# Kernel optimization log

Hardware: AMD Instinct MI355X
Metric: run time of the kernel (lower is better)

## Reference

```python
import jax, jax.numpy as jnp
import numpy as np

EPS = 1e-5


def setup_inputs() -> dict:
    key = jax.random.key(0)
    ks = jax.random.split(key, 10)
    B, C, H, W = 4, 256, 64, 64
    x = jax.random.normal(ks[0], (B, C, H, W), dtype=jnp.float32)
    s = 1.0 / np.sqrt(C)
    inp = {
        "x": x,
        "gn_w": jnp.ones((C,), jnp.float32),
        "gn_b": jnp.zeros((C,), jnp.float32),
        "wq": jax.random.normal(ks[1], (C, C), jnp.float32) * s,
        "bq": jnp.zeros((C,), jnp.float32),
        "wk": jax.random.normal(ks[2], (C, C), jnp.float32) * s,
        "bk": jnp.zeros((C,), jnp.float32),
        "wv": jax.random.normal(ks[3], (C, C), jnp.float32) * s,
        "bv": jnp.zeros((C,), jnp.float32),
        "wo": jax.random.normal(ks[4], (C, C), jnp.float32) * s,
        "bo": jnp.zeros((C,), jnp.float32),
    }
    return inp


def _forward(x, gn_w, gn_b, wq, bq, wk, bk, wv, bv, wo, bo):
    B, C, H, W = x.shape
    G = C // 2  # num_groups = channels // 2 -> 2 channels per group
    # GroupNorm
    xg = x.reshape(B, G, C // G, H, W)
    mu = jnp.mean(xg, axis=(2, 3, 4), keepdims=True)
    var = jnp.var(xg, axis=(2, 3, 4), keepdims=True)
    hn = ((xg - mu) * jax.lax.rsqrt(var + EPS)).reshape(B, C, H, W)
    hn = hn * gn_w[None, :, None, None] + gn_b[None, :, None, None]
    # tokens: (B, N, C), N = H*W
    h = hn.transpose(0, 2, 3, 1).reshape(B, H * W, C)
    q = h @ wq.T + bq
    k = h @ wk.T + bk
    v = h @ wv.T + bv
    # full NxN attention, scaled by C^-0.5 (as in original)
    scores = jnp.einsum("bnc,bmc->bnm", q, k) * (C ** -0.5)
    attn = jax.nn.softmax(scores, axis=-1)
    h2 = jnp.einsum("bnm,bmc->bnc", attn, v)  # (B, N, C)
    # faithful replication of the original's layout-scrambling reshape:
    # (B,N,C) -> (B,H,W,C) -> permute (B,C,H,W) -> reshape (B,HW,C)
    h2 = h2.reshape(B, H, W, C).transpose(0, 3, 1, 2).reshape(B, H * W, C)
    out = (h2 @ wo.T + bo).reshape(B, C, H, W)
    return x + out


def reference(x, gn_w, gn_b, wq, bq, wk, bk, wv, bv, wo, bo):
    return _forward(x, gn_w, gn_b, wq, bq, wk, bk, wv, bv, wo, bo)
```

## Files before the change

### kernel.cpp

```cpp
#include <hip/hip_runtime.h>

typedef unsigned short u16;
typedef unsigned int   u32;
typedef __attribute__((ext_vector_type(8)))  short short8;
typedef __attribute__((ext_vector_type(4)))  float f32x4;
typedef __attribute__((ext_vector_type(16))) float f32x16;

#define DI __device__ __forceinline__

DI u16 f2bf(float f){
  u32 u = __builtin_bit_cast(u32, f);
  u += 0x7fffu + ((u >> 16) & 1u);
  return (u16)(u >> 16);
}

DI void gl_lds16(const void* g, void* l){
  __builtin_amdgcn_global_load_lds((const __attribute__((address_space(1))) void*)g,
                                   (__attribute__((address_space(3))) void*)l, 16, 0, 0);
}

DI f32x4 mfma16(short8 a, short8 b, f32x4 c){
  return __builtin_amdgcn_mfma_f32_16x16x32_bf16(a, b, c, 0, 0, 0);
}
DI f32x16 mfma32(short8 a, short8 b, f32x16 c){
  return __builtin_amdgcn_mfma_f32_32x32x16_bf16(a, b, c, 0, 0, 0);
}
DI f32x16 z16(){
  f32x16 v;
  #pragma unroll
  for (int i=0;i<16;i++) v[i]=0.f;
  return v;
}

union U8 { u32 u[4]; short8 s; };

#define OFF_WBF   0u
#define OFF_STATS (512u<<10)
#define OFF_HTOK  (1u<<20)
#define OFF_Q     ((1u<<20) + (8u<<20))
#define OFF_K     ((1u<<20) + (16u<<20))
#define OFF_VT    ((1u<<20) + (24u<<20))
#define OFF_H2T   OFF_Q
#define OFF_PART  ((1u<<20) + (32u<<20))
#define OFF_ML    ((1u<<20) + (96u<<20))

__global__ void k_prep(const float* w0, const float* w1, const float* w2, const float* w3, u16* wbf){
  const float* src = (blockIdx.y==0)?w0:(blockIdx.y==1)?w1:(blockIdx.y==2)?w2:w3;
  u16* d = wbf + blockIdx.y*65536;
  int i = (blockIdx.x*256 + threadIdx.x)*4;
  float4 v = *(const float4*)(src + i);
  u32 lo = (u32)f2bf(v.x) | ((u32)f2bf(v.y)<<16);
  u32 hi = (u32)f2bf(v.z) | ((u32)f2bf(v.w)<<16);
  *(uint2*)(d + i) = make_uint2(lo, hi);
}

__global__ void k_gnstats(const float* x, float2* stats){
  int bg = blockIdx.x;
  const float* p = x + (size_t)bg*8192;
  float s = 0.f, ss = 0.f;
  #pragma unroll
  for (int i=0;i<8;i++){
    float4 v = *(const float4*)(p + threadIdx.x*4 + i*1024);
    s  += v.x+v.y+v.z+v.w;
    ss += v.x*v.x + v.y*v.y + v.z*v.z + v.w*v.w;
  }
  #pragma unroll
  for (int off=1; off<64; off<<=1){ s += __shfl_xor(s, off, 64); ss += __shfl_xor(ss, off, 64); }
  __shared__ float as[4], aq[4];
  int w = threadIdx.x>>6;
  if ((threadIdx.x&63)==0){ as[w]=s; aq[w]=ss; }
  __syncthreads();
  if (threadIdx.x==0){
    s = as[0]+as[1]+as[2]+as[3]; ss = aq[0]+aq[1]+aq[2]+aq[3];
    float mu = s * (1.f/8192.f);
    float var = ss * (1.f/8192.f) - mu*mu;
    stats[bg] = make_float2(mu, rsqrtf(var + 1e-5f));
  }
}

__global__ void k_gnapply(const float* x, const float* gw, const float* gb,
                          const float2* stats, u16* htok){
  __shared__ u16 tile[64*256];
  int b = blockIdx.y, n0 = blockIdx.x*64, t = threadIdx.x;
  const float* xb = x + (size_t)b*1048576;
  #pragma unroll
  for (int p=0;p<4;p++){
    int c = p*64 + (t>>2);
    float2 st = stats[b*128 + (c>>1)];
    float scl = st.y * gw[c];
    float off = gb[c] - st.x*scl;
    const float* src = xb + (size_t)c*4096 + n0 + (t&3)*16;
    #pragma unroll
    for (int u2=0;u2<4;u2++){
      float4 v = *(const float4*)(src + u2*4);
      float vv[4] = {v.x,v.y,v.z,v.w};
      #pragma unroll
      for (int j=0;j<4;j++){
        int n = (t&3)*16 + u2*4 + j;
        int addr = n*512 + ((c*2) ^ ((n&7)<<4));
        *(u16*)((char*)tile + addr) = f2bf(vv[j]*scl + off);
      }
    }
  }
  __syncthreads();
  int n = t>>2, seg = t&3;
  char* dst = (char*)(htok + ((size_t)(b*4096 + n0 + n)*256 + seg*64));
  #pragma unroll
  for (int i=0;i<8;i++){
    int boff = n*512 + (((seg*128) + i*16) ^ ((n&7)<<4));
    *(uint4*)(dst + i*16) = *(const uint4*)((const char*)tile + boff);
  }
}

__global__ __launch_bounds__(256,2) void k_qkv(const u16* htok, const u16* wbf,
    const float* bq, const float* bk, const float* bv,
    u16* qo, u16* ko, u16* vt){
  __shared__ u16 lds_a[64*256];
  const int t = threadIdx.x, row0 = blockIdx.x*64;
  const int w = t>>6, l = t&63, lo = l&15, hi = l>>4;
  {
    const char* Ab = (const char*)htok + (size_t)row0*512;
    #pragma unroll
    for (int i=0;i<8;i++){
      int row = w*16 + i*2 + (l>>5);
      gl_lds16(Ab + row*512 + (((l&31)*16) ^ ((row&7)<<4)), lds_a + w*4096 + i*512);
    }
    __syncthreads();
  }
  auto compute = [&](const u16* W, f32x4 acc[4][4]){
    #pragma unroll
    for (int i=0;i<4;i++)
      #pragma unroll
      for (int j=0;j<4;j++) acc[i][j] = (f32x4){0.f,0.f,0.f,0.f};
    const char* Wb = (const char*)W;
    #pragma unroll
    for (int dk=0; dk<4; dk++){
      #pragma unroll
      for (int s=0;s<2;s++){
        short8 af[4], bf[4];
        #pragma unroll
        for (int cf=0;cf<4;cf++){
          int col = w*64 + cf*16 + lo;
          bf[cf] = *(const short8*)(Wb + (size_t)col*512 + dk*128 + s*64 + hi*16);
        }
        #pragma unroll
        for (int rg=0;rg<4;rg++){
          int row = rg*16 + lo;
          af[rg] = *(const short8*)((const char*)lds_a + row*512 + ((dk*128 + s*64 + hi*16) ^ ((row&7)<<4)));
        }
        #pragma unroll
        for (int rg=0;rg<4;rg++)
          #pragma unroll
          for (int cf=0;cf<4;cf++)
            acc[rg][cf] = mfma16(af[rg], bf[cf], acc[rg][cf]);
      }
    }
  };
  f32x4 acc[4][4];
  compute(wbf, acc);
  #pragma unroll
  for (int rg=0;rg<4;rg++)
    #pragma unroll
    for (int cf=0;cf<4;cf++){
      int col = w*64 + cf*16 + lo;
      float bs = bq[col];
      #pragma unroll
      for (int r=0;r<4;r++){
        int grow = row0 + rg*16 + hi*4 + r;
        qo[(size_t)grow*256 + col] = f2bf((acc[rg][cf][r] + bs)*0.09016844f);
      }
    }
  compute(wbf + 65536, acc);
  #pragma unroll
  for (int rg=0;rg<4;rg++)
    #pragma unroll
    for (int cf=0;cf<4;cf++){
      int col = w*64 + cf*16 + lo;
      float bs = bk[col];
      #pragma unroll
      for (int r=0;r<4;r++){
        int grow = row0 + rg*16 + hi*4 + r;
        ko[(size_t)grow*256 + col] = f2bf(acc[rg][cf][r] + bs);
      }
    }
  compute(wbf + 2*65536, acc);
  __syncthreads();
  #pragma unroll
  for (int rg=0;rg<4;rg++)
    #pragma unroll
    for (int cf=0;cf<4;cf++){
      int col = w*64 + cf*16 + lo;
      float bs = bv[col];
      ushort4 pk;
      pk.x = f2bf(acc[rg][cf][0]+bs); pk.y = f2bf(acc[rg][cf][1]+bs);
      pk.z = f2bf(acc[rg][cf][2]+bs); pk.w = f2bf(acc[rg][cf][3]+bs);
      int rl = rg*16 + hi*4;
      int addr = col*128 + ((rl*2) ^ ((col&7)<<4));
      *(ushort4*)((char*)lds_a + addr) = pk;
    }
  __syncthreads();
  {
    int b = row0 >> 12, nb = row0 & 4095;
    #pragma unroll
    for (int p=0;p<8;p++){
      int c = p*32 + (t>>3), i = t&7;
      uint4 vd = *(const uint4*)((const char*)lds_a + c*128 + ((i*16) ^ ((c&7)<<4)));
      *(uint4*)((char*)vt + ((size_t)(b*256 + c)*4096 + nb)*2 + i*16) = vd;
    }
  }
}

__global__ __launch_bounds__(256,2) void k_out(const u16* h2t, const u16* wo,
    const float* bo, const float* x, float* out){
  __shared__ u16 lds_a[64*256];
  const int t = threadIdx.x, row0 = blockIdx.x*64;
  const int w = t>>6, l = t&63, lo = l&15, hi = l>>4;
  {
    const char* Ab = (const char*)h2t + (size_t)row0*512;
    #pragma unroll
    for (int i=0;i<8;i++){
      int row = w*16 + i*2 + (l>>5);
      gl_lds16(Ab + row*512 + (((l&31)*16) ^ ((row&7)<<4)), lds_a + w*4096 + i*512);
    }
    __syncthreads();
  }
  f32x4 acc[4][4];
  #pragma unroll
  for (int i=0;i<4;i++)
    #pragma unroll
    for (int j=0;j<4;j++) acc[i][j] = (f32x4){0.f,0.f,0.f,0.f};
  const char* Wb = (const char*)wo;
  #pragma unroll
  for (int dk=0; dk<4; dk++){
    #pragma unroll
    for (int s=0;s<2;s++){
      short8 af[4], bf[4];
      #pragma unroll
      for (int cf=0;cf<4;cf++){
        int col = w*64 + cf*16 + lo;
        bf[cf] = *(const short8*)(Wb + (size_t)col*512 + dk*128 + s*64 + hi*16);
      }
      #pragma unroll
      for (int rg=0;rg<4;rg++){
        int row = rg*16 + lo;
        af[rg] = *(const short8*)((const char*)lds_a + row*512 + ((dk*128 + s*64 + hi*16) ^ ((row&7)<<4)));
      }
      #pragma unroll
      for (int rg=0;rg<4;rg++)
        #pragma unroll
        for (int cf=0;cf<4;cf++)
          acc[rg][cf] = mfma16(af[rg], bf[cf], acc[rg][cf]);
    }
  }
  #pragma unroll
  for (int rg=0;rg<4;rg++)
    #pragma unroll
    for (int cf=0;cf<4;cf++){
      int col = w*64 + cf*16 + lo;
      float bs = bo[col];
      #pragma unroll
      for (int r=0;r<4;r++){
        size_t flat = (size_t)(row0 + rg*16 + hi*4 + r)*256 + col;
        out[flat] = x[flat] + acc[rg][cf][r] + bs;
      }
    }
}

__global__ __launch_bounds__(512,2) void k_attn(const u16* q, const u16* k,
                                                const u16* vt, u16* part, float2* ml){
  __shared__ char smem[131072];
  const int t = threadIdx.x, w = t>>6, l = t&63;
  const int lq = l&31, h = l>>5;
  const int bid = blockIdx.x;
  const int x = bid&7, idx = bid>>3;
  const int combo = x*2 + (idx&1);
  const int b = combo>>2, ks = combo&3, qt = idx>>1;

  const char* kg = (const char*)k  + ((size_t)b*4096 + (size_t)ks*1024)*512;
  const char* vg = (const char*)vt + (size_t)b*2097152 + (size_t)ks*2048;

  short8 qf[16];
  {
    const char* qrow = (const char*)q + ((size_t)b*4096 + qt*256 + w*32 + lq)*512;
    #pragma unroll
    for (int dk=0;dk<16;dk++) qf[dk] = *(const short8*)(qrow + dk*32 + h*16);
  }

  f32x16 O[8];
  #pragma unroll
  for (int ct=0;ct<8;ct++) O[ct] = z16();
  float m_run = -1e30f, l_run = 0.f;

  auto stage = [&](int sub){
    char* kd = smem + (sub&3)*16384;
    char* vd = smem + 65536 + (sub&3)*16384;
    #pragma unroll
    for (int j=0;j<2;j++){
      int key = w*4 + j*2 + h;
      gl_lds16(kg + (size_t)(sub*32 + key)*512 + (((l&31)*16) ^ ((key&7)<<4)),
               kd + (w*2+j)*1024);
    }
    #pragma unroll
    for (int j=0;j<2;j++){
      int c = w*32 + j*16 + (l>>2);
      gl_lds16(vg + (size_t)c*8192 + sub*64 + (((l&3)*16) ^ (((l>>3)&3)<<4)),
               vd + (w*2+j)*1024);
    }
  };

  auto qkt = [&](int sub, f32x16& S){
    const char* kbuf = smem + (sub&3)*16384;
    S = z16();
    #pragma unroll
    for (int dk=0;dk<16;dk++){
      short8 kf = *(const short8*)(kbuf + (size_t)lq*512 + ((dk*32 + h*16) ^ ((lq&7)<<4)));
      S = mfma32(kf, qf[dk], S);
    }
  };

  auto smpv = [&](int sub, const f32x16& S){
    const char* vbuf = smem + 65536 + (sub&3)*16384;
    float pmax = S[0];
    #pragma unroll
    for (int r=1;r<16;r++) pmax = fmaxf(pmax, S[r]);
    pmax = fmaxf(pmax, __shfl_xor(pmax, 32, 64));
    if (__any(pmax > m_run + 8.f)){
      float mn = fmaxf(m_run, pmax);
      float sclq = exp2f(m_run - mn);
      m_run = mn;
      l_run *= sclq;
      #pragma unroll
      for (int r=0;r<16;r++){
        float sr = __shfl(sclq, (r&3)+8*(r>>2)+4*h, 64);
        #pragma unroll
        for (int ct=0;ct<8;ct++) O[ct][r] *= sr;
      }
    }
    float p[16]; float ps = 0.f;
    #pragma unroll
    for (int r=0;r<16;r++){ p[r] = exp2f(S[r] - m_run); ps += p[r]; }
    l_run += ps + __shfl_xor(ps, 32, 64);
    u32 pk[8];
    #pragma unroll
    for (int j=0;j<8;j++){
      u32 u0 = __builtin_bit_cast(u32, p[2*j]);
      u32 u1 = __builtin_bit_cast(u32, p[2*j+1]);
      pk[j] = (u1 & 0xffff0000u) | (u0 >> 16);
    }
    #pragma unroll
    for (int kc=0;kc<2;kc++){
      u32 sA = h ? pk[4*kc]   : pk[4*kc+2];
      u32 sB = h ? pk[4*kc+1] : pk[4*kc+3];
      u32 xA = __shfl_xor(sA, 32, 64);
      u32 xB = __shfl_xor(sB, 32, 64);
      U8 pa;
      pa.u[0] = h ? xA : pk[4*kc];
      pa.u[1] = h ? xB : pk[4*kc+1];
      pa.u[2] = h ? pk[4*kc+2] : xA;
      pa.u[3] = h ? pk[4*kc+3] : xB;
      #pragma unroll
      for (int ct=0;ct<8;ct++){
        short8 vb = *(const short8*)(vbuf + (size_t)(ct*32+lq)*64 + ((kc*32 + h*16) ^ (((lq>>1)&3)<<4)));
        O[ct] = mfma32(pa.s, vb, O[ct]);
      }
    }
  };

  f32x16 SA, SB;
  stage(0); stage(1); stage(2);
  __syncthreads();
  qkt(0, SA);
  for (int it=0; it<30; it+=2){
    stage(it+3);
    qkt(it+1, SB);
    smpv(it, SA);
    __syncthreads();
    if (it+4 < 32) stage(it+4);
    qkt(it+2, SA);
    smpv(it+1, SB);
    __syncthreads();
  }
  qkt(31, SB);
  smpv(30, SA);
  smpv(31, SB);

  if (h == 0)
    ml[(size_t)combo*4096 + qt*256 + w*32 + lq] = make_float2(m_run, l_run);
  u16* otile = (u16*)smem;
  char* pbase = (char*)part + ((size_t)combo*4096 + (size_t)qt*256)*512;
  #pragma unroll
  for (int rd=0; rd<2; ++rd){
    __syncthreads();
    if ((w>>2) == rd){
      int wl = w&3;
      #pragma unroll
      for (int ct=0;ct<8;ct++)
        #pragma unroll
        for (int r=0;r<16;r++){
          int row = wl*32 + (r&3) + 8*(r>>2) + 4*h;
          otile[row*256 + ct*32 + lq] = f2bf(O[ct][r]);
        }
    }
    __syncthreads();
    const char* sb2 = (const char*)smem;
    char* gb2 = pbase + (size_t)rd*65536;
    #pragma unroll
    for (int j=0;j<8;j++)
      *(uint4*)(gb2 + t*16 + (size_t)j*8192) = *(const uint4*)(sb2 + t*16 + (size_t)j*8192);
  }
}

__global__ __launch_bounds__(256,2) void k_combine(const u16* part, const float2* ml, u16* h2t){
  __shared__ u16 tile[64*256];
  const int t = threadIdx.x, b = blockIdx.y, n0 = blockIdx.x*64;
  const int n = t>>2, cc = (t&3)*64;
  const int gn = n0 + n;
  float2 st[4]; float ms = -1e30f;
  #pragma unroll
  for (int ksi=0;ksi<4;ksi++){ st[ksi] = ml[(size_t)(b*4+ksi)*4096 + gn]; ms = fmaxf(ms, st[ksi].x); }
  float wn[4]; float denom = 0.f;
  #pragma unroll
  for (int ksi=0;ksi<4;ksi++){ wn[ksi] = exp2f(st[ksi].x - ms); denom += wn[ksi]*st[ksi].y; }
  float inv = 1.f/denom;
  #pragma unroll
  for (int ksi=0;ksi<4;ksi++) wn[ksi] *= inv;
  float acc[64];
  #pragma unroll
  for (int j=0;j<64;j++) acc[j] = 0.f;
  #pragma unroll
  for (int ksi=0;ksi<4;ksi++){
    const u16* src = part + ((size_t)(b*4+ksi)*4096 + gn)*256 + cc;
    float wv = wn[ksi];
    #pragma unroll
    for (int j8=0;j8<8;j8++){
      short8 v = *(const short8*)(src + j8*8);
      #pragma unroll
      for (int e=0;e<8;e++){
        u32 uu = ((u32)(u16)v[e])<<16;
        acc[j8*8+e] += wv * __builtin_bit_cast(float, uu);
      }
    }
  }
  char* tb = (char*)tile;
  #pragma unroll
  for (int j=0;j<32;j++){
    u32 pkv = ((u32)f2bf(acc[2*j+1])<<16) | f2bf(acc[2*j]);
    *(u32*)(tb + n*512 + ((cc*2 + j*4) ^ ((n&7)<<4))) = pkv;
  }
  __syncthreads();
  {
    const char* tbc = (const char*)tile;
    u32 outw[32];
    #pragma unroll
    for (int j=0;j<32;j++){
      u16 v0 = *(const u16*)(tbc + (2*j  )*512 + ((t*2) ^ (((2*j  )&7)<<4)));
      u16 v1 = *(const u16*)(tbc + (2*j+1)*512 + ((t*2) ^ (((2*j+1)&7)<<4)));
      outw[j] = ((u32)v1<<16) | v0;
    }
    char* dst = (char*)h2t + ((size_t)(b*256 + t)*4096 + n0)*2;
    #pragma unroll
    for (int j=0;j<8;j++){
      uint4 vv; vv.x = outw[4*j]; vv.y = outw[4*j+1]; vv.z = outw[4*j+2]; vv.w = outw[4*j+3];
      *(uint4*)(dst + j*16) = vv;
    }
  }
}

extern "C" void kernel_launch(void* const* d_in, const int* in_sizes, int n_in,
                              void* d_out, int out_size, void* d_ws, size_t ws_size,
                              hipStream_t stream) {
  const float* x    = (const float*)d_in[0];
  const float* gn_w = (const float*)d_in[1];
  const float* gn_b = (const float*)d_in[2];
  const float* wq   = (const float*)d_in[3];
  const float* bq   = (const float*)d_in[4];
  const float* wk   = (const float*)d_in[5];
  const float* bk   = (const float*)d_in[6];
  const float* wv   = (const float*)d_in[7];
  const float* bv   = (const float*)d_in[8];
  const float* wo   = (const float*)d_in[9];
  const float* bo   = (const float*)d_in[10];
  float* out = (float*)d_out;
  char* ws = (char*)d_ws;

  u16*    wbf   = (u16*)(ws + OFF_WBF);
  float2* stats = (float2*)(ws + OFF_STATS);
  u16*    htok  = (u16*)(ws + OFF_HTOK);
  u16*    qb    = (u16*)(ws + OFF_Q);
  u16*    kb    = (u16*)(ws + OFF_K);
  u16*    vt    = (u16*)(ws + OFF_VT);
  u16*    h2t   = (u16*)(ws + OFF_H2T);
  u16*    part  = (u16*)(ws + OFF_PART);
  float2* ml    = (float2*)(ws + OFF_ML);

  k_prep   <<<dim3(64,4), 256, 0, stream>>>(wq, wk, wv, wo, wbf);
  k_gnstats<<<512,        256, 0, stream>>>(x, stats);
  k_gnapply<<<dim3(64,4), 256, 0, stream>>>(x, gn_w, gn_b, stats, htok);
  k_qkv    <<<256,        256, 0, stream>>>(htok, wbf, bq, bk, bv, qb, kb, vt);
  k_attn   <<<256,        512, 0, stream>>>(qb, kb, vt, part, ml);
  k_combine<<<dim3(64,4), 256, 0, stream>>>(part, ml, h2t);
  k_out    <<<256,        256, 0, stream>>>(h2t, wbf + 3*65536, bo, x, out);
}
```

Before: 185.6 us.

## Restructure attention K/V pipeline into double-buffered 64-key tiles, merge prep kernels

```diff
diff --git a/kernel.cpp b/kernel.cpp
--- a/kernel.cpp
+++ b/kernel.cpp
@@ -44,18 +44,21 @@
 #define OFF_PART  ((1u<<20) + (32u<<20))
 #define OFF_ML    ((1u<<20) + (96u<<20))
 
-__global__ void k_prep(const float* w0, const float* w1, const float* w2, const float* w3, u16* wbf){
-  const float* src = (blockIdx.y==0)?w0:(blockIdx.y==1)?w1:(blockIdx.y==2)?w2:w3;
-  u16* d = wbf + blockIdx.y*65536;
-  int i = (blockIdx.x*256 + threadIdx.x)*4;
-  float4 v = *(const float4*)(src + i);
-  u32 lo = (u32)f2bf(v.x) | ((u32)f2bf(v.y)<<16);
-  u32 hi = (u32)f2bf(v.z) | ((u32)f2bf(v.w)<<16);
-  *(uint2*)(d + i) = make_uint2(lo, hi);
-}
-
-__global__ void k_gnstats(const float* x, float2* stats){
-  int bg = blockIdx.x;
+__global__ void k_prepstats(const float* wq, const float* wk, const float* wv, const float* wo,
+                            u16* wbf, const float* x, float2* stats){
+  const int bid = blockIdx.x;
+  if (bid < 256){
+    const int wi = bid >> 6;
+    const float* src = (wi==0)?wq:(wi==1)?wk:(wi==2)?wv:wo;
+    u16* d = wbf + wi*65536;
+    int i = ((bid&63)*256 + threadIdx.x)*4;
+    float4 v = *(const float4*)(src + i);
+    u32 lo = (u32)f2bf(v.x) | ((u32)f2bf(v.y)<<16);
+    u32 hi = (u32)f2bf(v.z) | ((u32)f2bf(v.w)<<16);
+    *(uint2*)(d + i) = make_uint2(lo, hi);
+    return;
+  }
+  const int bg = bid - 256;
   const float* p = x + (size_t)bg*8192;
   float s = 0.f, ss = 0.f;
   #pragma unroll
@@ -291,35 +294,27 @@
   for (int ct=0;ct<8;ct++) O[ct] = z16();
   float m_run = -1e30f, l_run = 0.f;
 
-  auto stage = [&](int sub){
-    char* kd = smem + (sub&3)*16384;
-    char* vd = smem + 65536 + (sub&3)*16384;
-    #pragma unroll
-    for (int j=0;j<2;j++){
-      int key = w*4 + j*2 + h;
-      gl_lds16(kg + (size_t)(sub*32 + key)*512 + (((l&31)*16) ^ ((key&7)<<4)),
-               kd + (w*2+j)*1024);
-    }
-    #pragma unroll
-    for (int j=0;j<2;j++){
-      int c = w*32 + j*16 + (l>>2);
-      gl_lds16(vg + (size_t)c*8192 + sub*64 + (((l&3)*16) ^ (((l>>3)&3)<<4)),
-               vd + (w*2+j)*1024);
+  auto stage = [&](int ti, int buf){
+    #pragma unroll
+    for (int sub=0; sub<2; ++sub){
+      char* kd = smem + buf*32768 + sub*16384;
+      char* vd = smem + 65536 + buf*32768 + sub*16384;
+      #pragma unroll
+      for (int j=0;j<2;j++){
+        int key = w*4 + j*2 + h;
+        gl_lds16(kg + (size_t)(ti*64 + sub*32 + key)*512 + (((l&31)*16) ^ ((key&7)<<4)),
+                 kd + (w*2+j)*1024);
+      }
+      #pragma unroll
+      for (int j=0;j<2;j++){
+        int c = w*32 + j*16 + (l>>2);
+        gl_lds16(vg + (size_t)c*8192 + ti*128 + sub*64 + (((l&3)*16) ^ (((l>>3)&3)<<4)),
+                 vd + (w*2+j)*1024);
+      }
     }
   };
 
-  auto qkt = [&](int sub, f32x16& S){
-    const char* kbuf = smem + (sub&3)*16384;
-    S = z16();
-    #pragma unroll
-    for (int dk=0;dk<16;dk++){
-      short8 kf = *(const short8*)(kbuf + (size_t)lq*512 + ((dk*32 + h*16) ^ ((lq&7)<<4)));
-      S = mfma32(kf, qf[dk], S);
-    }
-  };
-
-  auto smpv = [&](int sub, const f32x16& S){
-    const char* vbuf = smem + 65536 + (sub&3)*16384;
+  auto smpv = [&](const f32x16& S, const char* vbuf){
     float pmax = S[0];
     #pragma unroll
     for (int r=1;r<16;r++) pmax = fmaxf(pmax, S[r]);
@@ -358,31 +353,43 @@
       pa.u[1] = h ? xB : pk[4*kc+1];
       pa.u[2] = h ? pk[4*kc+2] : xA;
       pa.u[3] = h ? pk[4*kc+3] : xB;
+      __builtin_amdgcn_s_setprio(1);
       #pragma unroll
       for (int ct=0;ct<8;ct++){
         short8 vb = *(const short8*)(vbuf + (size_t)(ct*32+lq)*64 + ((kc*32 + h*16) ^ (((lq>>1)&3)<<4)));
         O[ct] = mfma32(pa.s, vb, O[ct]);
       }
+      __builtin_amdgcn_s_setprio(0);
     }
   };
 
-  f32x16 SA, SB;
-  stage(0); stage(1); stage(2);
+  stage(0, 0);
   __syncthreads();
-  qkt(0, SA);
-  for (int it=0; it<30; it+=2){
-    stage(it+3);
-    qkt(it+1, SB);
-    smpv(it, SA);
+
+  for (int tile=0; tile<16; ++tile){
+    const int cur = tile&1;
+    if (tile < 15) stage(tile+1, cur^1);
+    const char* kbuf0 = smem + cur*32768;
+    const char* kbuf1 = kbuf0 + 16384;
+    const char* vbuf0 = smem + 65536 + cur*32768;
+    const char* vbuf1 = vbuf0 + 16384;
+
+    f32x16 S0 = z16(), S1 = z16();
+    __builtin_amdgcn_s_setprio(1);
+    #pragma unroll
+    for (int dk=0;dk<16;dk++){
+      int dby = (dk*32 + h*16) ^ ((lq&7)<<4);
+      short8 k0 = *(const short8*)(kbuf0 + (size_t)lq*512 + dby);
+      short8 k1 = *(const short8*)(kbuf1 + (size_t)lq*512 + dby);
+      S0 = mfma32(k0, qf[dk], S0);
+      S1 = mfma32(k1, qf[dk], S1);
+    }
+    __builtin_amdgcn_s_setprio(0);
+
+    smpv(S0, vbuf0);
+    smpv(S1, vbuf1);
     __syncthreads();
-    if (it+4 < 32) stage(it+4);
-    qkt(it+2, SA);
-    smpv(it+1, SB);
-    __syncthreads();
-  }
-  qkt(31, SB);
-  smpv(30, SA);
-  smpv(31, SB);
+  }
 
   if (h == 0)
     ml[(size_t)combo*4096 + qt*256 + w*32 + lq] = make_float2(m_run, l_run);
@@ -493,11 +500,10 @@
   u16*    part  = (u16*)(ws + OFF_PART);
   float2* ml    = (float2*)(ws + OFF_ML);
 
-  k_prep   <<<dim3(64,4), 256, 0, stream>>>(wq, wk, wv, wo, wbf);
-  k_gnstats<<<512,        256, 0, stream>>>(x, stats);
-  k_gnapply<<<dim3(64,4), 256, 0, stream>>>(x, gn_w, gn_b, stats, htok);
-  k_qkv    <<<256,        256, 0, stream>>>(htok, wbf, bq, bk, bv, qb, kb, vt);
-  k_attn   <<<256,        512, 0, stream>>>(qb, kb, vt, part, ml);
-  k_combine<<<dim3(64,4), 256, 0, stream>>>(part, ml, h2t);
-  k_out    <<<256,        256, 0, stream>>>(h2t, wbf + 3*65536, bo, x, out);
-}
+  k_prepstats<<<768,      256, 0, stream>>>(wq, wk, wv, wo, wbf, x, stats);
+  k_gnapply  <<<dim3(64,4), 256, 0, stream>>>(x, gn_w, gn_b, stats, htok);
+  k_qkv      <<<256,      256, 0, stream>>>(htok, wbf, bq, bk, bv, qb, kb, vt);
+  k_attn     <<<256,      512, 0, stream>>>(qb, kb, vt, part, ml);
+  k_combine  <<<dim3(64,4), 256, 0, stream>>>(part, ml, h2t);
+  k_out      <<<256,      256, 0, stream>>>(h2t, wbf + 3*65536, bo, x, out);
+}
```

New measurement: 167.8 us. -9.6%, faster.
